# Optimization experiments

Hardware: AMD Instinct MI355X
Metric: run time of the kernel (lower is better)

The kernel has to match this reference:

```python
import jax, jax.numpy as jnp
import numpy as np

N, D, H = 4096, 128, 8

def setup_inputs() -> dict:
    key = jax.random.key(0)
    ks = jax.random.split(key, 7)
    xavier = float(np.sqrt(6.0 / (D + D)))  # xavier_uniform for [*, D, D]
    x = jax.random.normal(ks[0], (N, D), dtype=jnp.float32)
    W_k = jax.random.uniform(ks[1], (H, D, D), minval=-xavier, maxval=xavier, dtype=jnp.float32)
    W_q = jax.random.uniform(ks[2], (H, D, D), minval=-xavier, maxval=xavier, dtype=jnp.float32)
    W_v = jax.random.uniform(ks[3], (H, D, D), minval=-xavier, maxval=xavier, dtype=jnp.float32)
    W_m = jnp.ones((H,), dtype=jnp.float32)
    lim = float(1.0 / np.sqrt(D))  # default torch Linear init range
    Wg = jax.random.uniform(ks[4], (D, D), minval=-lim, maxval=lim, dtype=jnp.float32)
    bg = jax.random.uniform(ks[5], (D,), minval=-lim, maxval=lim, dtype=jnp.float32)
    return {"x": x, "W_k": W_k, "W_q": W_q, "W_v": W_v, "W_m": W_m, "Wg": Wg, "bg": bg}

def reference(x, W_k, W_q, W_v, W_m, Wg, bg):
    # per-head projections: [H, N, D]
    q = jnp.einsum('nf,hfd->hnd', x, W_q)
    k = jnp.einsum('nf,hfd->hnd', x, W_k)
    v = jnp.einsum('nf,hfd->hnd', x, W_v)
    # dense all-pairs attention scores per head: [H, N, N]
    e = jnp.einsum('hnd,hmd->hnm', q, k)
    attn = jax.nn.softmax(e, axis=-1)
    # weighted sum over values, then head-scaled accumulation: [N, D]
    out = jnp.einsum('h,hnm,hmd->nd', W_m, attn, v)
    # residual MLP: x + ReLU(Linear(x + out))
    h = x + out
    g = jax.nn.relu(h @ Wg.T + bg)
    return x + g
```

## Files before the change

kernel.cpp:

```cpp
#include <hip/hip_runtime.h>

#define NROWS 4096
#define DDIM  128
#define NHEAD 8
#define LOG2E 1.44269504088896f

extern "C" __device__ float __ocml_native_exp2_f32(float);

typedef __attribute__((ext_vector_type(8))) short    short8;
typedef __attribute__((ext_vector_type(8))) _Float16 half8;
typedef __attribute__((ext_vector_type(4))) float    floatx4;

__device__ __forceinline__ float bf2f(unsigned short u){
  unsigned v = ((unsigned)u) << 16;
  return __builtin_bit_cast(float, v);
}
__device__ __forceinline__ unsigned short f2bf(float f){
  unsigned u = __builtin_bit_cast(unsigned, f);
  u += 0x7FFFu + ((u >> 16) & 1u);
  return (unsigned short)(u >> 16);
}
__device__ __forceinline__ void split2(float v, unsigned short& hi, unsigned short& lo){
  hi = f2bf(v);
  lo = f2bf(v - bf2f(hi));
}
__device__ __forceinline__ void async_cp16(const _Float16* g, _Float16* l){
  __builtin_amdgcn_global_load_lds(
      (const __attribute__((address_space(1))) void*)g,
      (__attribute__((address_space(3))) void*)l, 16, 0, 0);
}

__global__ void fill_kernel(float* __restrict__ out, float val, int n){
  int i = blockIdx.x * 256 + threadIdx.x;
  if (i < n) out[i] = val;
}

__global__ __launch_bounds__(256, 2) void proj_kernel(
    const float* __restrict__ x,
    const float* __restrict__ Wk, const float* __restrict__ Wv,
    const float* __restrict__ Wq,
    _Float16* __restrict__ kfo, _Float16* __restrict__ vfo,
    _Float16* __restrict__ qfo)
{
  __shared__ alignas(16) unsigned short wthi[DDIM][72];
  __shared__ alignas(16) unsigned short wtlo[DDIM][72];
  const int tid = threadIdx.x, lane = tid & 63, wave = tid >> 6;
  const int l4 = lane & 15, quad = lane >> 4;
  const int h = blockIdx.y, z = blockIdx.z;
  const float* W = (z == 0 ? Wk : (z == 1 ? Wv : Wq)) + h * DDIM * DDIM;

  floatx4 acc[4][8];
#pragma unroll
  for (int t4 = 0; t4 < 4; t4++)
#pragma unroll
    for (int c = 0; c < 8; c++) acc[t4][c] = (floatx4)0.f;

  for (int fh = 0; fh < 2; fh++) {
    for (int i = tid; i < DDIM * 64; i += 256) {
      const int d = i & 127, fl = i >> 7;
      unsigned short hi, lo;
      split2(W[(fh * 64 + fl) * DDIM + d], hi, lo);
      wthi[d][fl] = hi; wtlo[d][fl] = lo;
    }
    __syncthreads();

#pragma unroll
    for (int t4 = 0; t4 < 4; t4++) {
      const int tile = blockIdx.x * 4 + t4;
      const float* xr = x + (size_t)(tile * 64 + wave * 16 + l4) * DDIM + fh * 64 + quad * 8;
      short8 ah[2], al[2];
#pragma unroll
      for (int t2 = 0; t2 < 2; t2++) {
        float4 v0 = *(const float4*)(xr + t2 * 32);
        float4 v1 = *(const float4*)(xr + t2 * 32 + 4);
        float xv[8] = {v0.x, v0.y, v0.z, v0.w, v1.x, v1.y, v1.z, v1.w};
#pragma unroll
        for (int j = 0; j < 8; j++) {
          unsigned short hi, lo; split2(xv[j], hi, lo);
          ah[t2][j] = (short)hi; al[t2][j] = (short)lo;
        }
      }
#pragma unroll
      for (int t2 = 0; t2 < 2; t2++) {
#pragma unroll
        for (int c = 0; c < 8; c++) {
          short8 bh = *(const short8*)(&wthi[c * 16 + l4][t2 * 32 + quad * 8]);
          short8 bl = *(const short8*)(&wtlo[c * 16 + l4][t2 * 32 + quad * 8]);
          acc[t4][c] = __builtin_amdgcn_mfma_f32_16x16x32_bf16(ah[t2], bh, acc[t4][c], 0, 0, 0);
          acc[t4][c] = __builtin_amdgcn_mfma_f32_16x16x32_bf16(al[t2], bh, acc[t4][c], 0, 0, 0);
          acc[t4][c] = __builtin_amdgcn_mfma_f32_16x16x32_bf16(ah[t2], bl, acc[t4][c], 0, 0, 0);
        }
      }
    }
    __syncthreads();
  }

  const int rb = wave * 16 + quad * 4;
#pragma unroll
  for (int t4 = 0; t4 < 4; t4++) {
    const int tile = blockIdx.x * 4 + t4;
    const size_t tilebase = (size_t)(h * 64 + tile) * 8192;
#pragma unroll
    for (int c = 0; c < 8; c++) {
      const int d = c * 16 + l4;
#pragma unroll
      for (int r = 0; r < 4; r++) {
        const int kl = rb + r;
        const float val = acc[t4][c][r];
        if (z == 0) {
          const int c2 = kl >> 4, l4k = kl & 15;
          const int tt = d >> 5, qd = (d >> 3) & 3, jj = d & 7;
          const int qX = qd ^ ((l4k >> 1) & 3);
          kfo[tilebase + (size_t)((c2 * 4 + tt) * 16 + l4k) * 32 + qX * 8 + jj] =
              (_Float16)val;
        } else if (z == 1) {
          const int c2 = d >> 4, l4v = d & 15;
          const int tt = kl >> 5, qd = (kl >> 3) & 3, jj = kl & 7;
          const int qX = qd ^ ((l4v >> 1) & 3);
          vfo[tilebase + (size_t)((c2 * 2 + tt) * 16 + l4v) * 32 + qX * 8 + jj] =
              (_Float16)val;
        } else {
          qfo[((size_t)h * NROWS + (size_t)tile * 64 + kl) * DDIM + d] =
              (_Float16)(val * LOG2E);
        }
      }
    }
  }
}

struct FlashLds {
  _Float16 k[2][8192];
  _Float16 p[4][1024];
};

__global__ __launch_bounds__(256, 3) void flash_kernel(
    const _Float16* __restrict__ qfo, const _Float16* __restrict__ kfo,
    const _Float16* __restrict__ vfo,
    _Float16* __restrict__ op, float* __restrict__ mb, float* __restrict__ lb)
{
  __shared__ alignas(16) FlashLds lds;
  const int tid = threadIdx.x, lane = tid & 63, wave = tid >> 6;
  const int l4 = lane & 15, quad = lane >> 4;
  const int h = blockIdx.x & 7, qt = (blockIdx.x >> 3) & 63, s = blockIdx.x >> 9;
  const int q0 = qt * 64;

  half8 aq[4];
  {
    const _Float16* qr =
        qfo + ((size_t)h * NROWS + q0 + wave * 16 + l4) * DDIM + quad * 8;
#pragma unroll
    for (int t = 0; t < 4; t++) aq[t] = *(const half8*)(qr + t * 32);
  }

  float m_run[4];
#pragma unroll
  for (int r = 0; r < 4; r++) m_run[r] = -1e30f;
  floatx4 Oacc[8], lacc = (floatx4)0.f;
#pragma unroll
  for (int c = 0; c < 8; c++) Oacc[c] = (floatx4)0.f;

  half8 vones;
#pragma unroll
  for (int j = 0; j < 8; j++) vones[j] = (_Float16)1.f;

  const _Float16* kfo_h = kfo + (size_t)h * 64 * 8192;
  const _Float16* vfo_h = vfo + (size_t)h * 64 * 8192;
  const int lq = (l4 * 4 + (quad ^ ((l4 >> 1) & 3))) * 8;
  const int kt0 = s * 32, kt1 = kt0 + 32;

  {
    const _Float16* ks = kfo_h + (size_t)kt0 * 8192 + wave * 2048 + lane * 8;
    _Float16* kd = &lds.k[0][wave * 2048];
#pragma unroll
    for (int it = 0; it < 4; it++) async_cp16(ks + it * 512, kd + it * 512);
  }

  for (int kt = kt0; kt < kt1; ++kt) {
    const int cur = kt & 1;
    __syncthreads();

    if (kt + 1 < kt1) {
      const _Float16* ks = kfo_h + (size_t)(kt + 1) * 8192 + wave * 2048 + lane * 8;
      _Float16* kd = &lds.k[cur ^ 1][wave * 2048];
#pragma unroll
      for (int it = 0; it < 4; it++) async_cp16(ks + it * 512, kd + it * 512);
    }

    floatx4 Sf[4];
#pragma unroll
    for (int c = 0; c < 4; c++) Sf[c] = (floatx4)0.f;
#pragma unroll
    for (int t = 0; t < 4; t++) {
      half8 b[4];
#pragma unroll
      for (int c = 0; c < 4; c++)
        b[c] = *(const half8*)&lds.k[cur][(c * 4 + t) * 512 + lq];
#pragma unroll
      for (int c = 0; c < 4; c++)
        Sf[c] = __builtin_amdgcn_mfma_f32_16x16x32_f16(aq[t], b[c], Sf[c], 0, 0, 0);
    }

    float alpha[4];
    {
      float mt[4];
#pragma unroll
      for (int r = 0; r < 4; r++)
        mt[r] = fmaxf(fmaxf(Sf[0][r], Sf[1][r]), fmaxf(Sf[2][r], Sf[3][r]));
#pragma unroll
      for (int mk = 1; mk <= 8; mk <<= 1)
#pragma unroll
        for (int r = 0; r < 4; r++) mt[r] = fmaxf(mt[r], __shfl_xor(mt[r], mk, 64));
#pragma unroll
      for (int r = 0; r < 4; r++) {
        const float mn = fmaxf(m_run[r], mt[r]);
        alpha[r] = __ocml_native_exp2_f32(m_run[r] - mn);
        m_run[r] = mn;
      }
#pragma unroll
      for (int r = 0; r < 4; r++)
#pragma unroll
        for (int c = 0; c < 4; c++)
          Sf[c][r] = __ocml_native_exp2_f32(Sf[c][r] - m_run[r]);
    }

#pragma unroll
    for (int c = 0; c < 4; c++)
#pragma unroll
      for (int r = 0; r < 4; r++)
        lds.p[wave][((c * 2 + (l4 >> 3)) * 16 + quad * 4 + r) * 8 + (l4 & 7)] =
            (_Float16)Sf[c][r];

    half8 vfrag[8][2];
    {
      const _Float16* vtb = vfo_h + (size_t)kt * 8192;
#pragma unroll
      for (int c = 0; c < 8; c++)
#pragma unroll
        for (int t = 0; t < 2; t++)
          vfrag[c][t] = *(const half8*)(vtb + (c * 2 + t) * 512 + lq);
    }

    {
      const bool moved = (alpha[0] != 1.f) | (alpha[1] != 1.f) |
                         (alpha[2] != 1.f) | (alpha[3] != 1.f);
      if (__any(moved)) {
#pragma unroll
        for (int c = 0; c < 8; c++) {
          Oacc[c][0] *= alpha[0]; Oacc[c][1] *= alpha[1];
          Oacc[c][2] *= alpha[2]; Oacc[c][3] *= alpha[3];
        }
        lacc[0] *= alpha[0]; lacc[1] *= alpha[1];
        lacc[2] *= alpha[2]; lacc[3] *= alpha[3];
      }
    }

#pragma unroll
    for (int t = 0; t < 2; t++) {
      half8 ap = *(const half8*)&lds.p[wave][((t * 4 + quad) * 16 + l4) * 8];
      lacc = __builtin_amdgcn_mfma_f32_16x16x32_f16(ap, vones, lacc, 0, 0, 0);
#pragma unroll
      for (int c = 0; c < 8; c++)
        Oacc[c] = __builtin_amdgcn_mfma_f32_16x16x32_f16(ap, vfrag[c][t], Oacc[c], 0, 0, 0);
    }
  }

  const int rbase = wave * 16 + quad * 4;
  const size_t rowbase = (size_t)(s * NHEAD + h) * NROWS + q0 + rbase;
#pragma unroll
  for (int c = 0; c < 8; c++) {
    const int col = c * 16 + l4;
#pragma unroll
    for (int r = 0; r < 4; r++)
      op[(rowbase + r) * DDIM + col] = (_Float16)Oacc[c][r];
  }
  if (l4 == 0) {
#pragma unroll
    for (int r = 0; r < 4; r++) {
      mb[rowbase + r] = m_run[r];
      lb[rowbase + r] = lacc[r];
    }
  }
}

__global__ __launch_bounds__(128) void merge_kernel(
    const _Float16* __restrict__ op, const float* __restrict__ mb,
    const float* __restrict__ lb, const float* __restrict__ Wm,
    float* __restrict__ u)
{
  __shared__ float sc[2][NHEAD];
  const int n = blockIdx.x, d = threadIdx.x;
  if (d < NHEAD) {
    const int h = d;
    const float m1 = mb[(size_t)h * NROWS + n];
    const float m2 = mb[(size_t)(NHEAD + h) * NROWS + n];
    const float l1 = lb[(size_t)h * NROWS + n];
    const float l2 = lb[(size_t)(NHEAD + h) * NROWS + n];
    const float m  = fmaxf(m1, m2);
    const float a1 = __ocml_native_exp2_f32(m1 - m);
    const float a2 = __ocml_native_exp2_f32(m2 - m);
    const float invL = Wm[h] / (l1 * a1 + l2 * a2);
    sc[0][h] = a1 * invL;
    sc[1][h] = a2 * invL;
  }
  __syncthreads();
  float acc = 0.f;
#pragma unroll
  for (int h = 0; h < NHEAD; h++) {
    acc += sc[0][h] * (float)op[((size_t)h * NROWS + n) * DDIM + d];
    acc += sc[1][h] * (float)op[((size_t)(NHEAD + h) * NROWS + n) * DDIM + d];
  }
  u[(size_t)n * DDIM + d] = acc;
}

__global__ __launch_bounds__(256, 2) void mlp_kernel(
    const float* __restrict__ x, const float* __restrict__ u,
    const float* __restrict__ Wg, const float* __restrict__ bg,
    float* __restrict__ out)
{
  __shared__ alignas(16) unsigned short wghi[DDIM][72];
  __shared__ alignas(16) unsigned short wglo[DDIM][72];
  const int tid = threadIdx.x, lane = tid & 63, wave = tid >> 6;
  const int l4 = lane & 15, quad = lane >> 4;
  const int r0 = blockIdx.x * 64;

  floatx4 acc[8];
#pragma unroll
  for (int c = 0; c < 8; c++) acc[c] = (floatx4)0.f;

  for (int fh = 0; fh < 2; fh++) {
    for (int i = tid; i < DDIM * 64; i += 256) {
      const int ii = i >> 6, jl = i & 63;
      unsigned short hi, lo;
      split2(Wg[ii * DDIM + fh * 64 + jl], hi, lo);
      wghi[ii][jl] = hi; wglo[ii][jl] = lo;
    }
    __syncthreads();

    const size_t xoff = (size_t)(r0 + wave * 16 + l4) * DDIM + fh * 64 + quad * 8;
    short8 ah[2], al[2];
#pragma unroll
    for (int t2 = 0; t2 < 2; t2++) {
      float4 x0 = *(const float4*)(x + xoff + t2 * 32);
      float4 x1 = *(const float4*)(x + xoff + t2 * 32 + 4);
      float4 u0 = *(const float4*)(u + xoff + t2 * 32);
      float4 u1 = *(const float4*)(u + xoff + t2 * 32 + 4);
      float hv[8] = {x0.x + u0.x, x0.y + u0.y, x0.z + u0.z, x0.w + u0.w,
                     x1.x + u1.x, x1.y + u1.y, x1.z + u1.z, x1.w + u1.w};
#pragma unroll
      for (int j = 0; j < 8; j++) {
        unsigned short hi, lo; split2(hv[j], hi, lo);
        ah[t2][j] = (short)hi; al[t2][j] = (short)lo;
      }
    }
#pragma unroll
    for (int t2 = 0; t2 < 2; t2++) {
#pragma unroll
      for (int c = 0; c < 8; c++) {
        short8 bh = *(const short8*)(&wghi[c * 16 + l4][t2 * 32 + quad * 8]);
        short8 bl = *(const short8*)(&wglo[c * 16 + l4][t2 * 32 + quad * 8]);
        acc[c] = __builtin_amdgcn_mfma_f32_16x16x32_bf16(ah[t2], bh, acc[c], 0, 0, 0);
        acc[c] = __builtin_amdgcn_mfma_f32_16x16x32_bf16(al[t2], bh, acc[c], 0, 0, 0);
        acc[c] = __builtin_amdgcn_mfma_f32_16x16x32_bf16(ah[t2], bl, acc[c], 0, 0, 0);
      }
    }
    __syncthreads();
  }

  const int rbase = wave * 16 + quad * 4;
#pragma unroll
  for (int c = 0; c < 8; c++) {
    const int col = c * 16 + l4;
    const float bgf = bg[col];
#pragma unroll
    for (int r = 0; r < 4; r++) {
      const size_t idx = (size_t)(r0 + rbase + r) * DDIM + col;
      out[idx] = x[idx] + fmaxf(acc[c][r] + bgf, 0.f);
    }
  }
}

extern "C" void kernel_launch(void* const* d_in, const int* in_sizes, int n_in,
                              void* d_out, int out_size, void* d_ws, size_t ws_size,
                              hipStream_t stream) {
  float* out = (float*)d_out;
  const int fill_blocks = (out_size + 255) / 256;

  const bool ok_sizes =
      n_in == 7 &&
      in_sizes[0] == NROWS * DDIM &&
      in_sizes[1] == NHEAD * DDIM * DDIM &&
      in_sizes[2] == NHEAD * DDIM * DDIM &&
      in_sizes[3] == NHEAD * DDIM * DDIM &&
      in_sizes[4] == NHEAD &&
      in_sizes[5] == DDIM * DDIM &&
      in_sizes[6] == DDIM &&
      out_size == NROWS * DDIM;
  if (!ok_sizes) {
    fill_kernel<<<fill_blocks, 256, 0, stream>>>(out, 1000.f, out_size);
    return;
  }

  const size_t HND = (size_t)NHEAD * NROWS * DDIM;
  const size_t ND  = (size_t)NROWS * DDIM;
  const size_t need = ND * 4 + 3 * HND * 2 + 2 * HND * 2 + 2 * NHEAD * NROWS * 8;
  if (ws_size < need) {
    fill_kernel<<<fill_blocks, 256, 0, stream>>>(out, 500.f, out_size);
    return;
  }

  const float* x  = (const float*)d_in[0];
  const float* Wk = (const float*)d_in[1];
  const float* Wq = (const float*)d_in[2];
  const float* Wv = (const float*)d_in[3];
  const float* Wm = (const float*)d_in[4];
  const float* Wg = (const float*)d_in[5];
  const float* bg = (const float*)d_in[6];

  float*     u   = (float*)d_ws;
  _Float16*  kfo = (_Float16*)(u + ND);
  _Float16*  vfo = kfo + HND;
  _Float16*  qfo = vfo + HND;
  _Float16*  op  = qfo + HND;
  float*     mb  = (float*)(op + 2 * HND);
  float*     lb  = mb + 2 * NHEAD * NROWS;

  (void)hipGetLastError();
  proj_kernel<<<dim3(16, NHEAD, 3), 256, 0, stream>>>(x, Wk, Wv, Wq, kfo, vfo, qfo);
  flash_kernel<<<dim3(1024), 256, 0, stream>>>(qfo, kfo, vfo, op, mb, lb);
  merge_kernel<<<dim3(4096), 128, 0, stream>>>(op, mb, lb, Wm, u);
  mlp_kernel<<<dim3(64), 256, 0, stream>>>(x, u, Wg, bg, out);
  if (hipGetLastError() != hipSuccess) {
    fill_kernel<<<fill_blocks, 256, 0, stream>>>(out, 2000.f, out_size);
  }
}
```

Before: 257.8 us.

## Presplit weights in prep kernel, split flash KV into three chunks, add setprio

A new prep kernel splits the weights and x into bf16 hi/lo pairs once, writing them in a swizzled layout. The projection and MLP kernels then load weight tiles with async global-to-LDS copies instead of converting in every block. The flash kernel now splits the keys into three chunks instead of two (1536 blocks) to improve CU occupancy and balance, and the merge kernel combines three partials. It also raises wave priority around the MFMA sections. The costs are one extra kernel launch, a larger workspace, and more partial-result traffic in merge.

```diff
diff --git a/kernel.cpp b/kernel.cpp
--- a/kernel.cpp
+++ b/kernel.cpp
@@ -24,7 +24,7 @@
   hi = f2bf(v);
   lo = f2bf(v - bf2f(hi));
 }
-__device__ __forceinline__ void async_cp16(const _Float16* g, _Float16* l){
+__device__ __forceinline__ void async_cp16(const void* g, void* l){
   __builtin_amdgcn_global_load_lds(
       (const __attribute__((address_space(1))) void*)g,
       (__attribute__((address_space(3))) void*)l, 16, 0, 0);
@@ -35,19 +35,74 @@
   if (i < n) out[i] = val;
 }
 
+__global__ __launch_bounds__(256) void prep_kernel(
+    const float* __restrict__ Wk, const float* __restrict__ Wv,
+    const float* __restrict__ Wq, const float* __restrict__ Wg,
+    const float* __restrict__ x,
+    unsigned short* __restrict__ wpre, unsigned short* __restrict__ wgpre,
+    unsigned short* __restrict__ xh, unsigned short* __restrict__ xl)
+{
+  const int id = blockIdx.x * 256 + threadIdx.x;
+  if (id < 49152) {
+    const int z = id >> 14, rem = id & 16383;
+    const int h = rem >> 11, rem2 = rem & 2047;
+    const int fh = rem2 >> 10, L = rem2 & 1023;
+    const int d = L >> 3, m = L & 7;
+    const int kk0 = (m ^ (d & 7)) << 3;
+    const float* W = (z == 0 ? Wk : (z == 1 ? Wv : Wq)) + h * DDIM * DDIM;
+    short8 hi8, lo8;
+#pragma unroll
+    for (int j = 0; j < 8; j++) {
+      unsigned short hi, lo;
+      split2(W[(fh * 64 + kk0 + j) * DDIM + d], hi, lo);
+      hi8[j] = (short)hi; lo8[j] = (short)lo;
+    }
+    unsigned short* base = wpre + (size_t)((z * 8 + h) * 2 + fh) * 16384;
+    *(short8*)(base + L * 8) = hi8;
+    *(short8*)(base + 8192 + L * 8) = lo8;
+  } else if (id < 51200) {
+    const int t = id - 49152;
+    const int fh = t >> 10, L = t & 1023;
+    const int d = L >> 3, m = L & 7;
+    const int kk0 = (m ^ (d & 7)) << 3;
+    short8 hi8, lo8;
+#pragma unroll
+    for (int j = 0; j < 8; j++) {
+      unsigned short hi, lo;
+      split2(Wg[d * DDIM + fh * 64 + kk0 + j], hi, lo);
+      hi8[j] = (short)hi; lo8[j] = (short)lo;
+    }
+    unsigned short* base = wgpre + fh * 16384;
+    *(short8*)(base + L * 8) = hi8;
+    *(short8*)(base + 8192 + L * 8) = lo8;
+  } else if (id < 116736) {
+    const int t = id - 51200;
+    const float* src = x + (size_t)t * 8;
+    float4 v0 = *(const float4*)src, v1 = *(const float4*)(src + 4);
+    float xv[8] = {v0.x, v0.y, v0.z, v0.w, v1.x, v1.y, v1.z, v1.w};
+    short8 hi8, lo8;
+#pragma unroll
+    for (int j = 0; j < 8; j++) {
+      unsigned short hi, lo; split2(xv[j], hi, lo);
+      hi8[j] = (short)hi; lo8[j] = (short)lo;
+    }
+    *(short8*)(xh + (size_t)t * 8) = hi8;
+    *(short8*)(xl + (size_t)t * 8) = lo8;
+  }
+}
+
 __global__ __launch_bounds__(256, 2) void proj_kernel(
-    const float* __restrict__ x,
-    const float* __restrict__ Wk, const float* __restrict__ Wv,
-    const float* __restrict__ Wq,
+    const unsigned short* __restrict__ xh, const unsigned short* __restrict__ xl,
+    const unsigned short* __restrict__ wpre,
     _Float16* __restrict__ kfo, _Float16* __restrict__ vfo,
     _Float16* __restrict__ qfo)
 {
-  __shared__ alignas(16) unsigned short wthi[DDIM][72];
-  __shared__ alignas(16) unsigned short wtlo[DDIM][72];
+  __shared__ alignas(16) unsigned short whi[8192];
+  __shared__ alignas(16) unsigned short wlo[8192];
   const int tid = threadIdx.x, lane = tid & 63, wave = tid >> 6;
   const int l4 = lane & 15, quad = lane >> 4;
   const int h = blockIdx.y, z = blockIdx.z;
-  const float* W = (z == 0 ? Wk : (z == 1 ? Wv : Wq)) + h * DDIM * DDIM;
+  const unsigned short* wb = wpre + (size_t)((z * 8 + h) * 2) * 16384;
 
   floatx4 acc[4][8];
 #pragma unroll
@@ -56,36 +111,37 @@
     for (int c = 0; c < 8; c++) acc[t4][c] = (floatx4)0.f;
 
   for (int fh = 0; fh < 2; fh++) {
-    for (int i = tid; i < DDIM * 64; i += 256) {
-      const int d = i & 127, fl = i >> 7;
-      unsigned short hi, lo;
-      split2(W[(fh * 64 + fl) * DDIM + d], hi, lo);
-      wthi[d][fl] = hi; wtlo[d][fl] = lo;
+    {
+      const unsigned short* src = wb + fh * 16384;
+      const unsigned short* sh = src + wave * 2048 + lane * 8;
+      const unsigned short* sl = src + 8192 + wave * 2048 + lane * 8;
+      unsigned short* dh = &whi[wave * 2048];
+      unsigned short* dl = &wlo[wave * 2048];
+#pragma unroll
+      for (int it = 0; it < 4; it++) {
+        async_cp16(sh + it * 512, dh + it * 512);
+        async_cp16(sl + it * 512, dl + it * 512);
+      }
     }
     __syncthreads();
 
 #pragma unroll
     for (int t4 = 0; t4 < 4; t4++) {
-      const int tile = blockIdx.x * 4 + t4;
-      const float* xr = x + (size_t)(tile * 64 + wave * 16 + l4) * DDIM + fh * 64 + quad * 8;
+      const int row = blockIdx.x * 256 + t4 * 64 + wave * 16 + l4;
+      const size_t xo = (size_t)row * DDIM + fh * 64 + quad * 8;
       short8 ah[2], al[2];
+      ah[0] = *(const short8*)(xh + xo);
+      ah[1] = *(const short8*)(xh + xo + 32);
+      al[0] = *(const short8*)(xl + xo);
+      al[1] = *(const short8*)(xl + xo + 32);
 #pragma unroll
       for (int t2 = 0; t2 < 2; t2++) {
-        float4 v0 = *(const float4*)(xr + t2 * 32);
-        float4 v1 = *(const float4*)(xr + t2 * 32 + 4);
-        float xv[8] = {v0.x, v0.y, v0.z, v0.w, v1.x, v1.y, v1.z, v1.w};
-#pragma unroll
-        for (int j = 0; j < 8; j++) {
-          unsigned short hi, lo; split2(xv[j], hi, lo);
-          ah[t2][j] = (short)hi; al[t2][j] = (short)lo;
-        }
-      }
-#pragma unroll
-      for (int t2 = 0; t2 < 2; t2++) {
 #pragma unroll
         for (int c = 0; c < 8; c++) {
-          short8 bh = *(const short8*)(&wthi[c * 16 + l4][t2 * 32 + quad * 8]);
-          short8 bl = *(const short8*)(&wtlo[c * 16 + l4][t2 * 32 + quad * 8]);
+          const int col = c * 16 + l4;
+          const int idx = (col * 8 + ((t2 * 4 + quad) ^ (col & 7))) * 8;
+          short8 bh = *(const short8*)&whi[idx];
+          short8 bl = *(const short8*)&wlo[idx];
           acc[t4][c] = __builtin_amdgcn_mfma_f32_16x16x32_bf16(ah[t2], bh, acc[t4][c], 0, 0, 0);
           acc[t4][c] = __builtin_amdgcn_mfma_f32_16x16x32_bf16(al[t2], bh, acc[t4][c], 0, 0, 0);
           acc[t4][c] = __builtin_amdgcn_mfma_f32_16x16x32_bf16(ah[t2], bl, acc[t4][c], 0, 0, 0);
@@ -166,11 +222,12 @@
   const _Float16* kfo_h = kfo + (size_t)h * 64 * 8192;
   const _Float16* vfo_h = vfo + (size_t)h * 64 * 8192;
   const int lq = (l4 * 4 + (quad ^ ((l4 >> 1) & 3))) * 8;
-  const int kt0 = s * 32, kt1 = kt0 + 32;
+  const int kt0 = (s == 0) ? 0 : (s == 1 ? 22 : 43);
+  const int kt1 = (s == 0) ? 22 : (s == 1 ? 43 : 64);
 
   {
     const _Float16* ks = kfo_h + (size_t)kt0 * 8192 + wave * 2048 + lane * 8;
-    _Float16* kd = &lds.k[0][wave * 2048];
+    _Float16* kd = &lds.k[kt0 & 1][wave * 2048];
 #pragma unroll
     for (int it = 0; it < 4; it++) async_cp16(ks + it * 512, kd + it * 512);
   }
@@ -189,6 +246,7 @@
     floatx4 Sf[4];
 #pragma unroll
     for (int c = 0; c < 4; c++) Sf[c] = (floatx4)0.f;
+    __builtin_amdgcn_s_setprio(1);
 #pragma unroll
     for (int t = 0; t < 4; t++) {
       half8 b[4];
@@ -199,6 +257,7 @@
       for (int c = 0; c < 4; c++)
         Sf[c] = __builtin_amdgcn_mfma_f32_16x16x32_f16(aq[t], b[c], Sf[c], 0, 0, 0);
     }
+    __builtin_amdgcn_s_setprio(0);
 
     float alpha[4];
     {
@@ -254,6 +313,7 @@
       }
     }
 
+    __builtin_amdgcn_s_setprio(1);
 #pragma unroll
     for (int t = 0; t < 2; t++) {
       half8 ap = *(const half8*)&lds.p[wave][((t * 4 + quad) * 16 + l4) * 8];
@@ -262,6 +322,7 @@
       for (int c = 0; c < 8; c++)
         Oacc[c] = __builtin_amdgcn_mfma_f32_16x16x32_f16(ap, vfrag[c][t], Oacc[c], 0, 0, 0);
     }
+    __builtin_amdgcn_s_setprio(0);
   }
 
   const int rbase = wave * 16 + quad * 4;
@@ -287,38 +348,42 @@
     const float* __restrict__ lb, const float* __restrict__ Wm,
     float* __restrict__ u)
 {
-  __shared__ float sc[2][NHEAD];
+  __shared__ float sc[3][NHEAD];
   const int n = blockIdx.x, d = threadIdx.x;
   if (d < NHEAD) {
     const int h = d;
-    const float m1 = mb[(size_t)h * NROWS + n];
-    const float m2 = mb[(size_t)(NHEAD + h) * NROWS + n];
-    const float l1 = lb[(size_t)h * NROWS + n];
-    const float l2 = lb[(size_t)(NHEAD + h) * NROWS + n];
-    const float m  = fmaxf(m1, m2);
+    float m0 = mb[(size_t)(0 * NHEAD + h) * NROWS + n];
+    float m1 = mb[(size_t)(1 * NHEAD + h) * NROWS + n];
+    float m2 = mb[(size_t)(2 * NHEAD + h) * NROWS + n];
+    float l0 = lb[(size_t)(0 * NHEAD + h) * NROWS + n];
+    float l1 = lb[(size_t)(1 * NHEAD + h) * NROWS + n];
+    float l2 = lb[(size_t)(2 * NHEAD + h) * NROWS + n];
+    const float m = fmaxf(fmaxf(m0, m1), m2);
+    const float a0 = __ocml_native_exp2_f32(m0 - m);
     const float a1 = __ocml_native_exp2_f32(m1 - m);
     const float a2 = __ocml_native_exp2_f32(m2 - m);
-    const float invL = Wm[h] / (l1 * a1 + l2 * a2);
-    sc[0][h] = a1 * invL;
-    sc[1][h] = a2 * invL;
+    const float invL = Wm[h] / (l0 * a0 + l1 * a1 + l2 * a2);
+    sc[0][h] = a0 * invL;
+    sc[1][h] = a1 * invL;
+    sc[2][h] = a2 * invL;
   }
   __syncthreads();
   float acc = 0.f;
 #pragma unroll
-  for (int h = 0; h < NHEAD; h++) {
-    acc += sc[0][h] * (float)op[((size_t)h * NROWS + n) * DDIM + d];
-    acc += sc[1][h] * (float)op[((size_t)(NHEAD + h) * NROWS + n) * DDIM + d];
-  }
+  for (int s = 0; s < 3; s++)
+#pragma unroll
+    for (int h = 0; h < NHEAD; h++)
+      acc += sc[s][h] * (float)op[((size_t)(s * NHEAD + h) * NROWS + n) * DDIM + d];
   u[(size_t)n * DDIM + d] = acc;
 }
 
 __global__ __launch_bounds__(256, 2) void mlp_kernel(
     const float* __restrict__ x, const float* __restrict__ u,
-    const float* __restrict__ Wg, const float* __restrict__ bg,
+    const unsigned short* __restrict__ wgpre, const float* __restrict__ bg,
     float* __restrict__ out)
 {
-  __shared__ alignas(16) unsigned short wghi[DDIM][72];
-  __shared__ alignas(16) unsigned short wglo[DDIM][72];
+  __shared__ alignas(16) unsigned short whi[8192];
+  __shared__ alignas(16) unsigned short wlo[8192];
   const int tid = threadIdx.x, lane = tid & 63, wave = tid >> 6;
   const int l4 = lane & 15, quad = lane >> 4;
   const int r0 = blockIdx.x * 64;
@@ -328,11 +393,17 @@
   for (int c = 0; c < 8; c++) acc[c] = (floatx4)0.f;
 
   for (int fh = 0; fh < 2; fh++) {
-    for (int i = tid; i < DDIM * 64; i += 256) {
-      const int ii = i >> 6, jl = i & 63;
-      unsigned short hi, lo;
-      split2(Wg[ii * DDIM + fh * 64 + jl], hi, lo);
-      wghi[ii][jl] = hi; wglo[ii][jl] = lo;
+    {
+      const unsigned short* src = wgpre + fh * 16384;
+      const unsigned short* sh = src + wave * 2048 + lane * 8;
+      const unsigned short* sl = src + 8192 + wave * 2048 + lane * 8;
+      unsigned short* dh = &whi[wave * 2048];
+      unsigned short* dl = &wlo[wave * 2048];
+#pragma unroll
+      for (int it = 0; it < 4; it++) {
+        async_cp16(sh + it * 512, dh + it * 512);
+        async_cp16(sl + it * 512, dl + it * 512);
+      }
     }
     __syncthreads();
 
@@ -356,8 +427,10 @@
     for (int t2 = 0; t2 < 2; t2++) {
 #pragma unroll
       for (int c = 0; c < 8; c++) {
-        short8 bh = *(const short8*)(&wghi[c * 16 + l4][t2 * 32 + quad * 8]);
-        short8 bl = *(const short8*)(&wglo[c * 16 + l4][t2 * 32 + quad * 8]);
+        const int col = c * 16 + l4;
+        const int idx = (col * 8 + ((t2 * 4 + quad) ^ (col & 7))) * 8;
+        short8 bh = *(const short8*)&whi[idx];
+        short8 bl = *(const short8*)&wlo[idx];
         acc[c] = __builtin_amdgcn_mfma_f32_16x16x32_bf16(ah[t2], bh, acc[c], 0, 0, 0);
         acc[c] = __builtin_amdgcn_mfma_f32_16x16x32_bf16(al[t2], bh, acc[c], 0, 0, 0);
         acc[c] = __builtin_amdgcn_mfma_f32_16x16x32_bf16(ah[t2], bl, acc[c], 0, 0, 0);
@@ -402,7 +475,11 @@
 
   const size_t HND = (size_t)NHEAD * NROWS * DDIM;
   const size_t ND  = (size_t)NROWS * DDIM;
-  const size_t need = ND * 4 + 3 * HND * 2 + 2 * HND * 2 + 2 * NHEAD * NROWS * 8;
+  const size_t WPRE_N  = (size_t)3 * 8 * 2 * 16384;
+  const size_t WGPRE_N = (size_t)2 * 16384;
+  const size_t need = ND * 4 + 3 * HND * 2 + 3 * HND * 2 +
+                      2 * (3 * (size_t)NHEAD * NROWS) * 4 +
+                      (WPRE_N + WGPRE_N + 2 * ND) * 2;
   if (ws_size < need) {
     fill_kernel<<<fill_blocks, 256, 0, stream>>>(out, 500.f, out_size);
     return;
@@ -416,19 +493,24 @@
   const float* Wg = (const float*)d_in[5];
   const float* bg = (const float*)d_in[6];
 
-  float*     u   = (float*)d_ws;
-  _Float16*  kfo = (_Float16*)(u + ND);
-  _Float16*  vfo = kfo + HND;
-  _Float16*  qfo = vfo + HND;
-  _Float16*  op  = qfo + HND;
-  float*     mb  = (float*)(op + 2 * HND);
-  float*     lb  = mb + 2 * NHEAD * NROWS;
+  float*          u     = (float*)d_ws;
+  _Float16*       kfo   = (_Float16*)(u + ND);
+  _Float16*       vfo   = kfo + HND;
+  _Float16*       qfo   = vfo + HND;
+  _Float16*       op    = qfo + HND;
+  float*          mb    = (float*)(op + 3 * HND);
+  float*          lb    = mb + 3 * NHEAD * NROWS;
+  unsigned short* wpre  = (unsigned short*)(lb + 3 * NHEAD * NROWS);
+  unsigned short* wgpre = wpre + WPRE_N;
+  unsigned short* xh    = wgpre + WGPRE_N;
+  unsigned short* xl    = xh + ND;
 
   (void)hipGetLastError();
-  proj_kernel<<<dim3(16, NHEAD, 3), 256, 0, stream>>>(x, Wk, Wv, Wq, kfo, vfo, qfo);
-  flash_kernel<<<dim3(1024), 256, 0, stream>>>(qfo, kfo, vfo, op, mb, lb);
+  prep_kernel<<<dim3(456), 256, 0, stream>>>(Wk, Wv, Wq, Wg, x, wpre, wgpre, xh, xl);
+  proj_kernel<<<dim3(16, NHEAD, 3), 256, 0, stream>>>(xh, xl, wpre, kfo, vfo, qfo);
+  flash_kernel<<<dim3(1536), 256, 0, stream>>>(qfo, kfo, vfo, op, mb, lb);
   merge_kernel<<<dim3(4096), 128, 0, stream>>>(op, mb, lb, Wm, u);
-  mlp_kernel<<<dim3(64), 256, 0, stream>>>(x, u, Wg, bg, out);
+  mlp_kernel<<<dim3(64), 256, 0, stream>>>(x, u, wgpre, bg, out);
   if (hipGetLastError() != hipSuccess) {
     fill_kernel<<<fill_blocks, 256, 0, stream>>>(out, 2000.f, out_size);
   }
```

Result: faster. 233.9 us (-9.3%).
